# Kernel tuning notes

Hardware: AMD Instinct MI355X
Metric: run time of the kernel (lower is better)

## Reference

```python
import jax, jax.numpy as jnp
import numpy as np

L = 0.05  # lx = ly = lz box half-extent

# 8 box corners [8,3]
_CORNERS = jnp.array([[sx * L, sy * L, sz * L]
                      for sx in (-1.0, 1.0) for sy in (-1.0, 1.0) for sz in (-1.0, 1.0)],
                     dtype=jnp.float32)
# match original ordering: [-,-,-],[-,-,+],[-,+,-],... which the comprehension above yields


def _euler_R(pose):
    """pose: [B,6] -> R [B,3,3], t [B,3] (yaw, pitch, roll convention from source)."""
    yaw, pitch, roll = pose[:, 0], pose[:, 1], pose[:, 2]
    cy, sy = jnp.cos(yaw), jnp.sin(yaw)
    cp, sp = jnp.cos(pitch), jnp.sin(pitch)
    cr, sr = jnp.cos(roll), jnp.sin(roll)
    R = jnp.stack([
        jnp.stack([cy * cp, cy * sp * sr - sy * cr, cy * sp * cr + sy * sr], axis=-1),
        jnp.stack([sy * cp, sy * sp * sr + cy * cr, sy * sp * cr - cy * sr], axis=-1),
        jnp.stack([-sp, cp * sr, cp * cr], axis=-1),
    ], axis=-2)  # [B,3,3]
    t = pose[:, 3:]  # [B,3]
    return R, t


def _transform_corners(pose):
    R, t = _euler_R(pose)
    # [B,8,3] = corners @ R^T + t
    return jnp.einsum('bij,nj->bni', R, _CORNERS) + t[:, None, :]


def setup_inputs() -> dict:
    key = jax.random.key(0)
    k1, k2, k3, k4 = jax.random.split(key, 4)
    B, C = 1048576, 16
    return {
        'pred_pose': jax.random.normal(k1, (B, 6), dtype=jnp.float32),
        'pred_class': jax.random.normal(k2, (B, C), dtype=jnp.float32),
        'target_pose': jax.random.normal(k3, (B, 6), dtype=jnp.float32),
        'target_class': jax.random.normal(k4, (B, C), dtype=jnp.float32),
    }


def reference(pred_pose, pred_class, target_pose, target_class):
    pts_pred = _transform_corners(pred_pose)    # [B,8,3]
    pts_gt = _transform_corners(target_pose)    # [B,8,3]
    # per-sample pose diff: mean over 8 corner L2 norms, then mean over batch
    norms = jnp.linalg.norm(pts_pred - pts_gt, axis=-1)  # [B,8]
    loss_pose = norms.mean(axis=-1).mean()
    class_loss = jnp.mean((pred_class - target_class) ** 2)
    total_loss = loss_pose + class_loss
    return total_loss, loss_pose, class_loss
```

## Files before the change

kernel.cpp:

```cpp
#include <hip/hip_runtime.h>
#include <math.h>

#define CORNER_L 0.05f

constexpr int THREADS = 256;
constexpr int BLOCKS  = 2048;

__device__ __forceinline__ float pose_elem(
    float py, float pp_, float pr, float ptx, float pty, float ptz,
    float ty, float tp_, float tr, float ttx, float tty, float ttz)
{
    float sy1 = __sinf(py),  cy1 = __cosf(py);
    float sp1 = __sinf(pp_), cp1 = __cosf(pp_);
    float sr1 = __sinf(pr),  cr1 = __cosf(pr);
    float sy2 = __sinf(ty),  cy2 = __cosf(ty);
    float sp2 = __sinf(tp_), cp2 = __cosf(tp_);
    float sr2 = __sinf(tr),  cr2 = __cosf(tr);

    float a0 = CORNER_L * (cy1 * cp1 - cy2 * cp2);
    float a1 = CORNER_L * ((cy1 * sp1 * sr1 - sy1 * cr1) - (cy2 * sp2 * sr2 - sy2 * cr2));
    float a2 = CORNER_L * ((cy1 * sp1 * cr1 + sy1 * sr1) - (cy2 * sp2 * cr2 + sy2 * sr2));
    float b0 = CORNER_L * (sy1 * cp1 - sy2 * cp2);
    float b1 = CORNER_L * ((sy1 * sp1 * sr1 + cy1 * cr1) - (sy2 * sp2 * sr2 + cy2 * cr2));
    float b2 = CORNER_L * ((sy1 * sp1 * cr1 - cy1 * sr1) - (sy2 * sp2 * cr2 - cy2 * sr2));
    float c0 = CORNER_L * (sp2 - sp1);
    float c1 = CORNER_L * (cp1 * sr1 - cp2 * sr2);
    float c2 = CORNER_L * (cp1 * cr1 - cp2 * cr2);
    float dtx = ptx - ttx;
    float dty = pty - tty;
    float dtz = ptz - ttz;

    float nsum = 0.0f;
    #pragma unroll
    for (int s = 0; s < 8; ++s) {
        float sx = (s & 4) ? 1.0f : -1.0f;
        float sy = (s & 2) ? 1.0f : -1.0f;
        float sz = (s & 1) ? 1.0f : -1.0f;
        float d0 = sx * a0 + sy * a1 + sz * a2 + dtx;
        float d1 = sx * b0 + sy * b1 + sz * b2 + dty;
        float d2 = sx * c0 + sy * c1 + sz * c2 + dtz;
        nsum += __builtin_amdgcn_sqrtf(d0 * d0 + d1 * d1 + d2 * d2);
    }
    return nsum;
}

__global__ __launch_bounds__(THREADS, 4) void pose_loss_reduce(
    const float4* __restrict__ pp4,
    const float4* __restrict__ pc4,
    const float4* __restrict__ tp4,
    const float4* __restrict__ tc4,
    float* __restrict__ ws, int B)
{
    const int tid  = threadIdx.x;
    const size_t gtid = (size_t)blockIdx.x * THREADS + tid;
    const size_t G    = (size_t)BLOCKS * THREADS;

    float class_acc = 0.0f;
    {
        float acc0 = 0.f, acc1 = 0.f, acc2 = 0.f, acc3 = 0.f;
        #pragma unroll
        for (int r = 0; r < 2; ++r) {
            const size_t base = gtid + (size_t)r * 4 * G;
            float4 p0 = pc4[base];
            float4 p1 = pc4[base + G];
            float4 p2 = pc4[base + 2 * G];
            float4 p3 = pc4[base + 3 * G];
            float4 t0 = tc4[base];
            float4 t1 = tc4[base + G];
            float4 t2 = tc4[base + 2 * G];
            float4 t3 = tc4[base + 3 * G];
            float dx, dy, dz, dw;
            dx = p0.x - t0.x; dy = p0.y - t0.y; dz = p0.z - t0.z; dw = p0.w - t0.w;
            acc0 += dx * dx + dy * dy + dz * dz + dw * dw;
            dx = p1.x - t1.x; dy = p1.y - t1.y; dz = p1.z - t1.z; dw = p1.w - t1.w;
            acc1 += dx * dx + dy * dy + dz * dz + dw * dw;
            dx = p2.x - t2.x; dy = p2.y - t2.y; dz = p2.z - t2.z; dw = p2.w - t2.w;
            acc2 += dx * dx + dy * dy + dz * dz + dw * dw;
            dx = p3.x - t3.x; dy = p3.y - t3.y; dz = p3.z - t3.z; dw = p3.w - t3.w;
            acc3 += dx * dx + dy * dy + dz * dz + dw * dw;
        }
        class_acc = (acc0 + acc1) + (acc2 + acc3);
    }

    float pose_acc = 0.0f;
    {
        const size_t f4 = gtid * 3;
        float4 P0 = pp4[f4], P1 = pp4[f4 + 1], P2 = pp4[f4 + 2];
        float4 T0 = tp4[f4], T1 = tp4[f4 + 1], T2 = tp4[f4 + 2];
        pose_acc += pose_elem(P0.x, P0.y, P0.z, P0.w, P1.x, P1.y,
                              T0.x, T0.y, T0.z, T0.w, T1.x, T1.y);
        pose_acc += pose_elem(P1.z, P1.w, P2.x, P2.y, P2.z, P2.w,
                              T1.z, T1.w, T2.x, T2.y, T2.z, T2.w);
    }

    #pragma unroll
    for (int off = 32; off > 0; off >>= 1) {
        pose_acc  += __shfl_down(pose_acc,  off);
        class_acc += __shfl_down(class_acc, off);
    }
    __shared__ float r_pose[4], r_class[4];
    const int lane = tid & 63;
    const int wave = tid >> 6;
    if (lane == 0) { r_pose[wave] = pose_acc; r_class[wave] = class_acc; }
    __syncthreads();
    if (tid == 0) {
        ws[2 * blockIdx.x]     = r_pose[0] + r_pose[1] + r_pose[2] + r_pose[3];
        ws[2 * blockIdx.x + 1] = r_class[0] + r_class[1] + r_class[2] + r_class[3];
    }
}

__global__ __launch_bounds__(THREADS) void pose_loss_finalize(
    const float* __restrict__ ws, float* __restrict__ out,
    int nblocks, float inv_pose, float inv_class)
{
    float p = 0.0f, c = 0.0f;
    for (int k = threadIdx.x; k < nblocks; k += THREADS) {
        p += ws[2 * k];
        c += ws[2 * k + 1];
    }
    #pragma unroll
    for (int off = 32; off > 0; off >>= 1) {
        p += __shfl_down(p, off);
        c += __shfl_down(c, off);
    }
    __shared__ float r_p[4], r_c[4];
    const int lane = threadIdx.x & 63;
    const int wave = threadIdx.x >> 6;
    if (lane == 0) { r_p[wave] = p; r_c[wave] = c; }
    __syncthreads();
    if (threadIdx.x == 0) {
        float lp = (r_p[0] + r_p[1] + r_p[2] + r_p[3]) * inv_pose;
        float lc = (r_c[0] + r_c[1] + r_c[2] + r_c[3]) * inv_class;
        out[0] = lp + lc;
        out[1] = lp;
        out[2] = lc;
    }
}

extern "C" void kernel_launch(void* const* d_in, const int* in_sizes, int n_in,
                              void* d_out, int out_size, void* d_ws, size_t ws_size,
                              hipStream_t stream) {
    const float4* pred_pose    = (const float4*)d_in[0];
    const float4* pred_class   = (const float4*)d_in[1];
    const float4* target_pose  = (const float4*)d_in[2];
    const float4* target_class = (const float4*)d_in[3];
    float* out = (float*)d_out;
    float* ws  = (float*)d_ws;

    const int B = in_sizes[0] / 6;

    pose_loss_reduce<<<BLOCKS, THREADS, 0, stream>>>(pred_pose, pred_class,
                                                     target_pose, target_class, ws, B);

    const float inv_pose  = 1.0f / (8.0f  * (float)B);
    const float inv_class = 1.0f / (16.0f * (float)B);
    pose_loss_finalize<<<1, THREADS, 0, stream>>>(ws, out, BLOCKS, inv_pose, inv_class);
}
```

Baseline: 189.0 us.

## Stage inputs through LDS with direct global-to-LDS loads and fuse finalize via atomics

Each block now stages contiguous tiles of class and pose data into shared memory with global_load_lds, then computes from LDS. This replaces the strided per-thread pose loads with coalesced tile loads. The separate finalize kernel is replaced by float atomics plus a last-block counter, with a memset to zero the workspace first. The costs are extra barriers, only half the threads doing pose math, a memset launch, and float atomic ordering making the sum nondeterministic.

```diff
diff --git a/kernel.cpp b/kernel.cpp
--- a/kernel.cpp
+++ b/kernel.cpp
@@ -4,7 +4,8 @@
 #define CORNER_L 0.05f
 
 constexpr int THREADS = 256;
-constexpr int BLOCKS  = 2048;
+constexpr int BLOCKS  = 4096;
+constexpr int TILE_E  = 128;
 
 __device__ __forceinline__ float pose_elem(
     float py, float pp_, float pr, float ptx, float pty, float ptz,
@@ -44,53 +45,62 @@
     return nsum;
 }
 
-__global__ __launch_bounds__(THREADS, 4) void pose_loss_reduce(
+__global__ __launch_bounds__(THREADS) void pose_loss_fused(
     const float4* __restrict__ pp4,
     const float4* __restrict__ pc4,
     const float4* __restrict__ tp4,
     const float4* __restrict__ tc4,
-    float* __restrict__ ws, int B)
+    float* __restrict__ ws,
+    float* __restrict__ out,
+    float inv_pose, float inv_class)
 {
+    __shared__ float4 sbuf[1408];
     const int tid  = threadIdx.x;
-    const size_t gtid = (size_t)blockIdx.x * THREADS + tid;
-    const size_t G    = (size_t)BLOCKS * THREADS;
+    const int lane = tid & 63;
+    const int wave = tid >> 6;
 
     float class_acc = 0.0f;
-    {
-        float acc0 = 0.f, acc1 = 0.f, acc2 = 0.f, acc3 = 0.f;
-        #pragma unroll
-        for (int r = 0; r < 2; ++r) {
-            const size_t base = gtid + (size_t)r * 4 * G;
-            float4 p0 = pc4[base];
-            float4 p1 = pc4[base + G];
-            float4 p2 = pc4[base + 2 * G];
-            float4 p3 = pc4[base + 3 * G];
-            float4 t0 = tc4[base];
-            float4 t1 = tc4[base + G];
-            float4 t2 = tc4[base + 2 * G];
-            float4 t3 = tc4[base + 3 * G];
+    float pose_acc  = 0.0f;
+
+    for (int it = 0; it < 2; ++it) {
+        const size_t tile  = (size_t)blockIdx.x * 2 + it;
+        const size_t cbase = tile * 512;
+        const size_t pbase = tile * 192;
+
+        for (int p = wave; p < 22; p += 4) {
+            const float4* src;
+            int soff;
+            if (p < 8)       { src = pc4 + cbase + (p << 6);        soff = (p << 6); }
+            else if (p < 16) { src = tc4 + cbase + ((p - 8) << 6);  soff = 512  + ((p - 8)  << 6); }
+            else if (p < 19) { src = pp4 + pbase + ((p - 16) << 6); soff = 1024 + ((p - 16) << 6); }
+            else             { src = tp4 + pbase + ((p - 19) << 6); soff = 1216 + ((p - 19) << 6); }
+            __builtin_amdgcn_global_load_lds(
+                (const __attribute__((address_space(1))) void*)(src + lane),
+                (__attribute__((address_space(3))) void*)(&sbuf[soff]),
+                16, 0, 0);
+        }
+        __syncthreads();
+
+        {
+            float4 a0 = sbuf[tid];        float4 b0 = sbuf[512 + tid];
+            float4 a1 = sbuf[256 + tid];  float4 b1 = sbuf[768 + tid];
             float dx, dy, dz, dw;
-            dx = p0.x - t0.x; dy = p0.y - t0.y; dz = p0.z - t0.z; dw = p0.w - t0.w;
-            acc0 += dx * dx + dy * dy + dz * dz + dw * dw;
-            dx = p1.x - t1.x; dy = p1.y - t1.y; dz = p1.z - t1.z; dw = p1.w - t1.w;
-            acc1 += dx * dx + dy * dy + dz * dz + dw * dw;
-            dx = p2.x - t2.x; dy = p2.y - t2.y; dz = p2.z - t2.z; dw = p2.w - t2.w;
-            acc2 += dx * dx + dy * dy + dz * dz + dw * dw;
-            dx = p3.x - t3.x; dy = p3.y - t3.y; dz = p3.z - t3.z; dw = p3.w - t3.w;
-            acc3 += dx * dx + dy * dy + dz * dz + dw * dw;
+            dx = a0.x - b0.x; dy = a0.y - b0.y; dz = a0.z - b0.z; dw = a0.w - b0.w;
+            class_acc += dx * dx + dy * dy + dz * dz + dw * dw;
+            dx = a1.x - b1.x; dy = a1.y - b1.y; dz = a1.z - b1.z; dw = a1.w - b1.w;
+            class_acc += dx * dx + dy * dy + dz * dz + dw * dw;
         }
-        class_acc = (acc0 + acc1) + (acc2 + acc3);
-    }
 
-    float pose_acc = 0.0f;
-    {
-        const size_t f4 = gtid * 3;
-        float4 P0 = pp4[f4], P1 = pp4[f4 + 1], P2 = pp4[f4 + 2];
-        float4 T0 = tp4[f4], T1 = tp4[f4 + 1], T2 = tp4[f4 + 2];
-        pose_acc += pose_elem(P0.x, P0.y, P0.z, P0.w, P1.x, P1.y,
-                              T0.x, T0.y, T0.z, T0.w, T1.x, T1.y);
-        pose_acc += pose_elem(P1.z, P1.w, P2.x, P2.y, P2.z, P2.w,
-                              T1.z, T1.w, T2.x, T2.y, T2.z, T2.w);
+        if (tid < TILE_E) {
+            const float* sf = (const float*)sbuf;
+            const int e6p = 4096 + tid * 6;
+            const int e6t = 4864 + tid * 6;
+            pose_acc += pose_elem(sf[e6p], sf[e6p + 1], sf[e6p + 2],
+                                  sf[e6p + 3], sf[e6p + 4], sf[e6p + 5],
+                                  sf[e6t], sf[e6t + 1], sf[e6t + 2],
+                                  sf[e6t + 3], sf[e6t + 4], sf[e6t + 5]);
+        }
+        __syncthreads();
     }
 
     #pragma unroll
@@ -99,41 +109,23 @@
         class_acc += __shfl_down(class_acc, off);
     }
     __shared__ float r_pose[4], r_class[4];
-    const int lane = tid & 63;
-    const int wave = tid >> 6;
     if (lane == 0) { r_pose[wave] = pose_acc; r_class[wave] = class_acc; }
     __syncthreads();
+
     if (tid == 0) {
-        ws[2 * blockIdx.x]     = r_pose[0] + r_pose[1] + r_pose[2] + r_pose[3];
-        ws[2 * blockIdx.x + 1] = r_class[0] + r_class[1] + r_class[2] + r_class[3];
-    }
-}
-
-__global__ __launch_bounds__(THREADS) void pose_loss_finalize(
-    const float* __restrict__ ws, float* __restrict__ out,
-    int nblocks, float inv_pose, float inv_class)
-{
-    float p = 0.0f, c = 0.0f;
-    for (int k = threadIdx.x; k < nblocks; k += THREADS) {
-        p += ws[2 * k];
-        c += ws[2 * k + 1];
-    }
-    #pragma unroll
-    for (int off = 32; off > 0; off >>= 1) {
-        p += __shfl_down(p, off);
-        c += __shfl_down(c, off);
-    }
-    __shared__ float r_p[4], r_c[4];
-    const int lane = threadIdx.x & 63;
-    const int wave = threadIdx.x >> 6;
-    if (lane == 0) { r_p[wave] = p; r_c[wave] = c; }
-    __syncthreads();
-    if (threadIdx.x == 0) {
-        float lp = (r_p[0] + r_p[1] + r_p[2] + r_p[3]) * inv_pose;
-        float lc = (r_c[0] + r_c[1] + r_c[2] + r_c[3]) * inv_class;
-        out[0] = lp + lc;
-        out[1] = lp;
-        out[2] = lc;
+        float bp = r_pose[0] + r_pose[1] + r_pose[2] + r_pose[3];
+        float bc = r_class[0] + r_class[1] + r_class[2] + r_class[3];
+        atomicAdd(&ws[0], bp);
+        atomicAdd(&ws[1], bc);
+        __threadfence();
+        unsigned old = atomicAdd((unsigned*)(ws + 2), 1u);
+        if (old == (unsigned)(gridDim.x - 1)) {
+            float lp = atomicAdd(&ws[0], 0.0f) * inv_pose;
+            float lc = atomicAdd(&ws[1], 0.0f) * inv_class;
+            out[0] = lp + lc;
+            out[1] = lp;
+            out[2] = lc;
+        }
     }
 }
 
@@ -149,10 +141,12 @@
 
     const int B = in_sizes[0] / 6;
 
-    pose_loss_reduce<<<BLOCKS, THREADS, 0, stream>>>(pred_pose, pred_class,
-                                                     target_pose, target_class, ws, B);
+    hipMemsetAsync(ws, 0, 4 * sizeof(float), stream);
 
     const float inv_pose  = 1.0f / (8.0f  * (float)B);
     const float inv_class = 1.0f / (16.0f * (float)B);
-    pose_loss_finalize<<<1, THREADS, 0, stream>>>(ws, out, BLOCKS, inv_pose, inv_class);
+
+    pose_loss_fused<<<BLOCKS, THREADS, 0, stream>>>(pred_pose, pred_class,
+                                                    target_pose, target_class,
+                                                    ws, out, inv_pose, inv_class);
 }
```

Result: slower. 384.0 us (+103.1%).

## Split fused class/pose reduction into separate kernels with nontemporal loads

Applied to the files above, without the earlier changes.

Replaces the single fused reduction kernel with two kernels: a grid-stride class MSE kernel and a pose-corner kernel, each writing partials to separate workspace regions that the finalize kernel sums. All global loads become nontemporal. The aim is simpler per-kernel register use and streaming loads that do not pollute the cache. In exchange it adds an extra kernel launch and loses the overlap of compute-heavy pose work with bandwidth-heavy class loads within one kernel.

```diff
diff --git a/kernel.cpp b/kernel.cpp
--- a/kernel.cpp
+++ b/kernel.cpp
@@ -3,8 +3,33 @@
 
 #define CORNER_L 0.05f
 
+typedef float f4 __attribute__((ext_vector_type(4)));
+
 constexpr int THREADS = 256;
-constexpr int BLOCKS  = 2048;
+constexpr int CBLOCKS = 2048;
+constexpr int PBLOCKS = 2048;
+
+__global__ __launch_bounds__(THREADS) void class_mse_kernel(
+    const f4* __restrict__ pc4, const f4* __restrict__ tc4,
+    float* __restrict__ ws, int n4)
+{
+    const int tid = threadIdx.x;
+    const size_t G = (size_t)CBLOCKS * THREADS;
+    float acc = 0.0f;
+    for (size_t i = (size_t)blockIdx.x * THREADS + tid; i < (size_t)n4; i += G) {
+        f4 p = __builtin_nontemporal_load(pc4 + i);
+        f4 t = __builtin_nontemporal_load(tc4 + i);
+        f4 d = p - t;
+        acc += d.x * d.x + d.y * d.y + d.z * d.z + d.w * d.w;
+    }
+    #pragma unroll
+    for (int off = 32; off > 0; off >>= 1) acc += __shfl_down(acc, off);
+    __shared__ float r[4];
+    const int lane = tid & 63, wave = tid >> 6;
+    if (lane == 0) r[wave] = acc;
+    __syncthreads();
+    if (tid == 0) ws[blockIdx.x] = r[0] + r[1] + r[2] + r[3];
+}
 
 __device__ __forceinline__ float pose_elem(
     float py, float pp_, float pr, float ptx, float pty, float ptz,
@@ -44,88 +69,50 @@
     return nsum;
 }
 
-__global__ __launch_bounds__(THREADS, 4) void pose_loss_reduce(
-    const float4* __restrict__ pp4,
-    const float4* __restrict__ pc4,
-    const float4* __restrict__ tp4,
-    const float4* __restrict__ tc4,
-    float* __restrict__ ws, int B)
+__global__ __launch_bounds__(THREADS) void pose_kernel(
+    const f4* __restrict__ pp4, const f4* __restrict__ tp4,
+    float* __restrict__ ws)
 {
-    const int tid  = threadIdx.x;
+    const int tid = threadIdx.x;
     const size_t gtid = (size_t)blockIdx.x * THREADS + tid;
-    const size_t G    = (size_t)BLOCKS * THREADS;
+    const size_t f = gtid * 3;
 
-    float class_acc = 0.0f;
-    {
-        float acc0 = 0.f, acc1 = 0.f, acc2 = 0.f, acc3 = 0.f;
-        #pragma unroll
-        for (int r = 0; r < 2; ++r) {
-            const size_t base = gtid + (size_t)r * 4 * G;
-            float4 p0 = pc4[base];
-            float4 p1 = pc4[base + G];
-            float4 p2 = pc4[base + 2 * G];
-            float4 p3 = pc4[base + 3 * G];
-            float4 t0 = tc4[base];
-            float4 t1 = tc4[base + G];
-            float4 t2 = tc4[base + 2 * G];
-            float4 t3 = tc4[base + 3 * G];
-            float dx, dy, dz, dw;
-            dx = p0.x - t0.x; dy = p0.y - t0.y; dz = p0.z - t0.z; dw = p0.w - t0.w;
-            acc0 += dx * dx + dy * dy + dz * dz + dw * dw;
-            dx = p1.x - t1.x; dy = p1.y - t1.y; dz = p1.z - t1.z; dw = p1.w - t1.w;
-            acc1 += dx * dx + dy * dy + dz * dz + dw * dw;
-            dx = p2.x - t2.x; dy = p2.y - t2.y; dz = p2.z - t2.z; dw = p2.w - t2.w;
-            acc2 += dx * dx + dy * dy + dz * dz + dw * dw;
-            dx = p3.x - t3.x; dy = p3.y - t3.y; dz = p3.z - t3.z; dw = p3.w - t3.w;
-            acc3 += dx * dx + dy * dy + dz * dz + dw * dw;
-        }
-        class_acc = (acc0 + acc1) + (acc2 + acc3);
-    }
+    f4 P0 = __builtin_nontemporal_load(pp4 + f);
+    f4 P1 = __builtin_nontemporal_load(pp4 + f + 1);
+    f4 P2 = __builtin_nontemporal_load(pp4 + f + 2);
+    f4 T0 = __builtin_nontemporal_load(tp4 + f);
+    f4 T1 = __builtin_nontemporal_load(tp4 + f + 1);
+    f4 T2 = __builtin_nontemporal_load(tp4 + f + 2);
 
-    float pose_acc = 0.0f;
-    {
-        const size_t f4 = gtid * 3;
-        float4 P0 = pp4[f4], P1 = pp4[f4 + 1], P2 = pp4[f4 + 2];
-        float4 T0 = tp4[f4], T1 = tp4[f4 + 1], T2 = tp4[f4 + 2];
-        pose_acc += pose_elem(P0.x, P0.y, P0.z, P0.w, P1.x, P1.y,
-                              T0.x, T0.y, T0.z, T0.w, T1.x, T1.y);
-        pose_acc += pose_elem(P1.z, P1.w, P2.x, P2.y, P2.z, P2.w,
-                              T1.z, T1.w, T2.x, T2.y, T2.z, T2.w);
-    }
+    float acc = 0.0f;
+    acc += pose_elem(P0.x, P0.y, P0.z, P0.w, P1.x, P1.y,
+                     T0.x, T0.y, T0.z, T0.w, T1.x, T1.y);
+    acc += pose_elem(P1.z, P1.w, P2.x, P2.y, P2.z, P2.w,
+                     T1.z, T1.w, T2.x, T2.y, T2.z, T2.w);
 
     #pragma unroll
-    for (int off = 32; off > 0; off >>= 1) {
-        pose_acc  += __shfl_down(pose_acc,  off);
-        class_acc += __shfl_down(class_acc, off);
-    }
-    __shared__ float r_pose[4], r_class[4];
-    const int lane = tid & 63;
-    const int wave = tid >> 6;
-    if (lane == 0) { r_pose[wave] = pose_acc; r_class[wave] = class_acc; }
+    for (int off = 32; off > 0; off >>= 1) acc += __shfl_down(acc, off);
+    __shared__ float r[4];
+    const int lane = tid & 63, wave = tid >> 6;
+    if (lane == 0) r[wave] = acc;
     __syncthreads();
-    if (tid == 0) {
-        ws[2 * blockIdx.x]     = r_pose[0] + r_pose[1] + r_pose[2] + r_pose[3];
-        ws[2 * blockIdx.x + 1] = r_class[0] + r_class[1] + r_class[2] + r_class[3];
-    }
+    if (tid == 0) ws[CBLOCKS + blockIdx.x] = r[0] + r[1] + r[2] + r[3];
 }
 
 __global__ __launch_bounds__(THREADS) void pose_loss_finalize(
     const float* __restrict__ ws, float* __restrict__ out,
-    int nblocks, float inv_pose, float inv_class)
+    float inv_pose, float inv_class)
 {
-    float p = 0.0f, c = 0.0f;
-    for (int k = threadIdx.x; k < nblocks; k += THREADS) {
-        p += ws[2 * k];
-        c += ws[2 * k + 1];
-    }
+    float c = 0.0f, p = 0.0f;
+    for (int k = threadIdx.x; k < CBLOCKS; k += THREADS) c += ws[k];
+    for (int k = threadIdx.x; k < PBLOCKS; k += THREADS) p += ws[CBLOCKS + k];
     #pragma unroll
     for (int off = 32; off > 0; off >>= 1) {
         p += __shfl_down(p, off);
         c += __shfl_down(c, off);
     }
     __shared__ float r_p[4], r_c[4];
-    const int lane = threadIdx.x & 63;
-    const int wave = threadIdx.x >> 6;
+    const int lane = threadIdx.x & 63, wave = threadIdx.x >> 6;
     if (lane == 0) { r_p[wave] = p; r_c[wave] = c; }
     __syncthreads();
     if (threadIdx.x == 0) {
@@ -140,19 +127,20 @@
 extern "C" void kernel_launch(void* const* d_in, const int* in_sizes, int n_in,
                               void* d_out, int out_size, void* d_ws, size_t ws_size,
                               hipStream_t stream) {
-    const float4* pred_pose    = (const float4*)d_in[0];
-    const float4* pred_class   = (const float4*)d_in[1];
-    const float4* target_pose  = (const float4*)d_in[2];
-    const float4* target_class = (const float4*)d_in[3];
+    const f4* pred_pose    = (const f4*)d_in[0];
+    const f4* pred_class   = (const f4*)d_in[1];
+    const f4* target_pose  = (const f4*)d_in[2];
+    const f4* target_class = (const f4*)d_in[3];
     float* out = (float*)d_out;
     float* ws  = (float*)d_ws;
 
-    const int B = in_sizes[0] / 6;
+    const int B  = in_sizes[0] / 6;
+    const int n4 = B * 4;
 
-    pose_loss_reduce<<<BLOCKS, THREADS, 0, stream>>>(pred_pose, pred_class,
-                                                     target_pose, target_class, ws, B);
+    class_mse_kernel<<<CBLOCKS, THREADS, 0, stream>>>(pred_class, target_class, ws, n4);
+    pose_kernel<<<PBLOCKS, THREADS, 0, stream>>>(pred_pose, target_pose, ws);
 
     const float inv_pose  = 1.0f / (8.0f  * (float)B);
     const float inv_class = 1.0f / (16.0f * (float)B);
-    pose_loss_finalize<<<1, THREADS, 0, stream>>>(ws, out, BLOCKS, inv_pose, inv_class);
+    pose_loss_finalize<<<1, THREADS, 0, stream>>>(ws, out, inv_pose, inv_class);
 }
```

Measured after the change: 180.1 us. 1.05x faster.
